# Optimization experiments

Hardware: AMD Instinct MI355X
Metric: run time of the kernel (lower is better)

Reference implementation:

```python
import jax, jax.numpy as jnp
import numpy as np

K = 9  # kernel_size (knn neighbors, loop=True -> self included)

def setup_inputs() -> dict:
    key = jax.random.key(0)
    k1, k2, k3 = jax.random.split(key, 3)
    B, C, H, W = 8, 64, 32, 32
    OUT = 64
    x = jax.random.normal(k1, (B, C, H, W), dtype=jnp.float32)
    # SAGEConv params: lin_l (neighbor aggregate, with bias), lin_r (root, no bias)
    s = 1.0 / np.sqrt(C)
    W_l = jax.random.uniform(k2, (OUT, C), minval=-s, maxval=s, dtype=jnp.float32)
    b_l = jnp.zeros((OUT,), dtype=jnp.float32)
    W_r = jax.random.uniform(k3, (OUT, C), minval=-s, maxval=s, dtype=jnp.float32)
    return {"x": x, "W_l": W_l, "b_l": b_l, "W_r": W_r}

def _knn_mean(x_f, batches):
    # squared-euclidean pairwise distances [N, N], masked across batches
    sq = jnp.sum(x_f * x_f, axis=-1)
    dist = sq[:, None] + sq[None, :] - 2.0 * (x_f @ x_f.T)
    cross = batches[:, None] != batches[None, :]
    dist = jnp.where(cross, jnp.inf, dist)
    neg, idx = jax.lax.top_k(-dist, K)          # k nearest (self included, dist 0)
    valid = (neg != -jnp.inf).astype(x_f.dtype)  # handle degenerate last-batch node
    nbr = x_f[idx] * valid[..., None]            # [N, K, C]
    return nbr.sum(axis=1) / valid.sum(axis=1, keepdims=True)

def reference(x, W_l, b_l, W_r):
    B, C, H, Wd = x.shape
    N = B * H * Wd
    x_f = x.transpose(0, 2, 3, 1).reshape(N, C)  # flat_nodes: [B*H*W, C]
    # torch.linspace(0, B, steps=N).to(int64): truncation of i*B/(N-1)
    batches = jnp.linspace(0.0, float(B), N).astype(jnp.int32)
    mean_nbr = _knn_mean(x_f, batches)
    # SAGEConv: lin_l(mean_j x_j) + lin_r(x_i)
    return mean_nbr @ W_l.T + b_l + x_f @ W_r.T
```

## Files before the change

### kernel.cpp

```cpp
#include <hip/hip_runtime.h>
#include <cstdint>
#include <cstddef>


__global__ __launch_bounds__(256, 2) void k_all(const float* __restrict__ x,
                                                const float* __restrict__ Wl,
                                                const float* __restrict__ bl,
                                                const float* __restrict__ Wr,
                                                float* __restrict__ out) {
  __shared__ float SH[8320];
  float4* Asf4 = (float4*)SH;

  int bi = (int)blockIdx.x, t = threadIdx.x;
  int lane = t & 63, w = t >> 6;
  int n0 = bi << 4;
  int s = (n0 >= 7168) ? 7168 : (n0 & ~1023);
  const float* xb = x + ((size_t)(s >> 10) << 16);
  const float* xrow = x + ((size_t)(n0 >> 10) << 16) + (n0 & 1023);

  {
    int ch = t >> 2, g = t & 3;
    Asf4[t] = *(const float4*)&xrow[((size_t)ch << 10) + (g << 2)];
  }
  __syncthreads();

  float4 av = Asf4[(lane << 2) + w];

  float acc[4][16];
  float sqa[16];
#pragma unroll
  for (int r = 0; r < 4; ++r)
#pragma unroll
    for (int j = 0; j < 16; ++j) acc[r][j] = 0.f;
#pragma unroll
  for (int j = 0; j < 16; ++j) sqa[j] = 0.f;

  const float* xl = xb + (lane << 2);
#pragma unroll 4
  for (int ch = 0; ch < 64; ++ch) {
    float4 a4 = Asf4[(ch << 2) + w];
    const float* xc = xl + ((size_t)ch << 10);
    float4 b0 = *(const float4*)&xc[0];
    float4 b1 = *(const float4*)&xc[256];
    float4 b2 = *(const float4*)&xc[512];
    float4 b3 = *(const float4*)&xc[768];
    float bv[16] = {b0.x, b0.y, b0.z, b0.w, b1.x, b1.y, b1.z, b1.w,
                    b2.x, b2.y, b2.z, b2.w, b3.x, b3.y, b3.z, b3.w};
    float ar[4] = {a4.x, a4.y, a4.z, a4.w};
#pragma unroll
    for (int j = 0; j < 16; ++j) {
      sqa[j] = fmaf(bv[j], bv[j], sqa[j]);
      acc[0][j] = fmaf(ar[0], bv[j], acc[0][j]);
      acc[1][j] = fmaf(ar[1], bv[j], acc[1][j]);
      acc[2][j] = fmaf(ar[2], bv[j], acc[2][j]);
      acc[3][j] = fmaf(ar[3], bv[j], acc[3][j]);
    }
  }

  float msum[4];
  int cnt[4];
#pragma unroll 4
  for (int rr = 0; rr < 4; ++rr) {
    int n = n0 + (w << 2) + rr;
    float xself = (rr == 0) ? av.x : (rr == 1) ? av.y : (rr == 2) ? av.z : av.w;
    if (n == 8191) {
      msum[rr] = xself;
      cnt[rr] = 1;
    } else {
      cnt[rr] = 9;
      int ln = n - s;
      int slot_o = ((ln >> 8) << 2) | (ln & 3);
      float sv = sqa[0];
#pragma unroll
      for (int j = 1; j < 16; ++j) sv = (slot_o == j) ? sqa[j] : sv;
      float si = __int_as_float(
          __builtin_amdgcn_readlane(__float_as_int(sv), (ln & 255) >> 2));
      bool mlast = (n >= 7168);
      unsigned long long cand[16];
#pragma unroll
      for (int q = 0; q < 4; ++q) {
#pragma unroll
        for (int e = 0; e < 4; ++e) {
          float d = (si + sqa[(q << 2) + e]) - 2.f * acc[rr][(q << 2) + e];
          unsigned u = __float_as_uint(d);
          u = (u & 0x80000000u) ? ~u : (u | 0x80000000u);
          unsigned jj = (unsigned)((q << 8) + (lane << 2) + e);
          cand[(q << 2) + e] = ((unsigned long long)u << 32) | jj;
        }
      }
      if (mlast && lane == 63) cand[15] = ~0ull;
      unsigned long long m1 = cand[0], m2 = cand[1];
      if (m2 < m1) { unsigned long long tt = m1; m1 = m2; m2 = tt; }
#pragma unroll
      for (int q = 2; q < 16; ++q) {
        unsigned long long c = cand[q];
        unsigned long long lo = (c < m1) ? c : m1;
        unsigned long long hi = (c < m1) ? m1 : c;
        m2 = (hi < m2) ? hi : m2;
        m1 = lo;
      }
      unsigned long long lm = m1;
      unsigned rmask = 0;
      bool stale = false;
      unsigned jloc[9];
#pragma unroll
      for (int kk = 0; kk < 9; ++kk) {
        unsigned long long g = lm;
#pragma unroll
        for (int off = 32; off; off >>= 1) {
          unsigned ghi = __shfl_xor((unsigned)(g >> 32), off, 64);
          unsigned glo = __shfl_xor((unsigned)g, off, 64);
          unsigned long long o = ((unsigned long long)ghi << 32) | glo;
          g = (o < g) ? o : g;
        }
        jloc[kk] = (unsigned)g & 1023u;
        if (lm == g) {
          unsigned slot = (((unsigned)g >> 6) & 12u) | ((unsigned)g & 3u);
          rmask |= 1u << slot;
          if (!stale) { lm = m2; stale = true; }
          else {
            unsigned long long best = ~0ull;
#pragma unroll
            for (int q = 0; q < 16; ++q) {
              bool alive = ((rmask >> q) & 1u) == 0u;
              unsigned long long c = cand[q];
              best = (alive && c < best) ? c : best;
            }
            lm = best;
          }
        }
      }
      const float* gx = xb + ((size_t)lane << 10);
      float g0 = gx[jloc[0]], g1 = gx[jloc[1]], g2 = gx[jloc[2]];
      float g3 = gx[jloc[3]], g4 = gx[jloc[4]], g5 = gx[jloc[5]];
      float g6 = gx[jloc[6]], g7 = gx[jloc[7]], g8 = gx[jloc[8]];
      msum[rr] = (((g0 + g1) + (g2 + g3)) + ((g4 + g5) + (g6 + g7))) + g8;
    }
  }
  __syncthreads();

#pragma unroll
  for (int i = 0; i < 16; ++i) {
    int lin = t + (i << 8);
    int o = lin >> 6, c = lin & 63;
    SH[o * 65 + c] = Wl[lin];
    SH[4160 + o * 65 + c] = Wr[lin];
  }
  __syncthreads();

  float bias = bl[lane];
  float ms[4];
#pragma unroll
  for (int rr = 0; rr < 4; ++rr)
    ms[rr] = (cnt[rr] == 9) ? msum[rr] * (1.f / 9.f) : msum[rr];
  float xr[4] = {av.x, av.y, av.z, av.w};
  float accL[4] = {0.f, 0.f, 0.f, 0.f};
  float accR[4] = {0.f, 0.f, 0.f, 0.f};
#pragma unroll
  for (int c = 0; c < 64; ++c) {
    float wlc = SH[lane * 65 + c];
    float wrc = SH[4160 + lane * 65 + c];
#pragma unroll
    for (int rr = 0; rr < 4; ++rr) {
      float mc = __int_as_float(__builtin_amdgcn_readlane(__float_as_int(ms[rr]), c));
      float xc = __int_as_float(__builtin_amdgcn_readlane(__float_as_int(xr[rr]), c));
      accL[rr] = fmaf(mc, wlc, accL[rr]);
      accR[rr] = fmaf(xc, wrc, accR[rr]);
    }
  }
#pragma unroll
  for (int rr = 0; rr < 4; ++rr)
    __builtin_nontemporal_store(accL[rr] + accR[rr] + bias,
                                &out[((size_t)(n0 + (w << 2) + rr) << 6) + lane]);
}

extern "C" void kernel_launch(void* const* d_in, const int* in_sizes, int n_in,
                              void* d_out, int out_size, void* d_ws, size_t ws_size,
                              hipStream_t stream) {
  const float* x  = (const float*)d_in[0];
  const float* Wl = (const float*)d_in[1];
  const float* bl = (const float*)d_in[2];
  const float* Wr = (const float*)d_in[3];
  float* out = (float*)d_out;
  (void)d_ws; (void)ws_size;

  k_all<<<dim3(512), 256, 0, stream>>>(x, Wl, bl, Wr, out);
}
```

Before: 107.0 us.

## Double-buffer distance loads and interleave top-k shuffle reductions across four rows

The distance GEMM loop now double-buffers global loads of two channels at a time in registers, so loads for the next pair overlap the FMAs on the current pair. The top-k selection handles all four rows together: the nine shuffle reductions of the four rows are interleaved to add instruction-level parallelism. Candidate keys are recomputed on demand instead of being kept in a 16-entry array, and the special-case row is handled by a select at the end. The cost is higher register pressure and extra recomputation in the rescan path.

```diff
diff --git a/kernel.cpp b/kernel.cpp
--- a/kernel.cpp
+++ b/kernel.cpp
@@ -2,6 +2,8 @@
 #include <cstdint>
 #include <cstddef>
 
+
+typedef unsigned long long u64;
 
 __global__ __launch_bounds__(256, 2) void k_all(const float* __restrict__ x,
                                                 const float* __restrict__ Wl,
@@ -36,106 +38,169 @@
   for (int j = 0; j < 16; ++j) sqa[j] = 0.f;
 
   const float* xl = xb + (lane << 2);
-#pragma unroll 4
-  for (int ch = 0; ch < 64; ++ch) {
-    float4 a4 = Asf4[(ch << 2) + w];
-    const float* xc = xl + ((size_t)ch << 10);
-    float4 b0 = *(const float4*)&xc[0];
-    float4 b1 = *(const float4*)&xc[256];
-    float4 b2 = *(const float4*)&xc[512];
-    float4 b3 = *(const float4*)&xc[768];
-    float bv[16] = {b0.x, b0.y, b0.z, b0.w, b1.x, b1.y, b1.z, b1.w,
-                    b2.x, b2.y, b2.z, b2.w, b3.x, b3.y, b3.z, b3.w};
-    float ar[4] = {a4.x, a4.y, a4.z, a4.w};
-#pragma unroll
-    for (int j = 0; j < 16; ++j) {
-      sqa[j] = fmaf(bv[j], bv[j], sqa[j]);
-      acc[0][j] = fmaf(ar[0], bv[j], acc[0][j]);
-      acc[1][j] = fmaf(ar[1], bv[j], acc[1][j]);
-      acc[2][j] = fmaf(ar[2], bv[j], acc[2][j]);
-      acc[3][j] = fmaf(ar[3], bv[j], acc[3][j]);
+
+#define LOADB(BUF, CH) do {                                                  \
+    const float* xc0_ = xl + ((size_t)(CH) << 10);                           \
+    const float* xc1_ = xl + ((size_t)((CH) + 1) << 10);                     \
+    BUF[0] = *(const float4*)&xc0_[0];   BUF[1] = *(const float4*)&xc0_[256];\
+    BUF[2] = *(const float4*)&xc0_[512]; BUF[3] = *(const float4*)&xc0_[768];\
+    BUF[4] = *(const float4*)&xc1_[0];   BUF[5] = *(const float4*)&xc1_[256];\
+    BUF[6] = *(const float4*)&xc1_[512]; BUF[7] = *(const float4*)&xc1_[768];\
+  } while (0)
+
+#define FMA2(BUF, CH) do {                                                   \
+    float4 a0_ = Asf4[((CH) << 2) + w];                                      \
+    float4 a1_ = Asf4[(((CH) + 1) << 2) + w];                                \
+    float bv0_[16] = {BUF[0].x, BUF[0].y, BUF[0].z, BUF[0].w,                \
+                      BUF[1].x, BUF[1].y, BUF[1].z, BUF[1].w,                \
+                      BUF[2].x, BUF[2].y, BUF[2].z, BUF[2].w,                \
+                      BUF[3].x, BUF[3].y, BUF[3].z, BUF[3].w};               \
+    _Pragma("unroll")                                                        \
+    for (int j_ = 0; j_ < 16; ++j_) {                                        \
+      float bv_ = bv0_[j_];                                                  \
+      sqa[j_] = fmaf(bv_, bv_, sqa[j_]);                                     \
+      acc[0][j_] = fmaf(a0_.x, bv_, acc[0][j_]);                             \
+      acc[1][j_] = fmaf(a0_.y, bv_, acc[1][j_]);                             \
+      acc[2][j_] = fmaf(a0_.z, bv_, acc[2][j_]);                             \
+      acc[3][j_] = fmaf(a0_.w, bv_, acc[3][j_]);                             \
+    }                                                                        \
+    float bv1_[16] = {BUF[4].x, BUF[4].y, BUF[4].z, BUF[4].w,                \
+                      BUF[5].x, BUF[5].y, BUF[5].z, BUF[5].w,                \
+                      BUF[6].x, BUF[6].y, BUF[6].z, BUF[6].w,                \
+                      BUF[7].x, BUF[7].y, BUF[7].z, BUF[7].w};               \
+    _Pragma("unroll")                                                        \
+    for (int j_ = 0; j_ < 16; ++j_) {                                        \
+      float bv_ = bv1_[j_];                                                  \
+      sqa[j_] = fmaf(bv_, bv_, sqa[j_]);                                     \
+      acc[0][j_] = fmaf(a1_.x, bv_, acc[0][j_]);                             \
+      acc[1][j_] = fmaf(a1_.y, bv_, acc[1][j_]);                             \
+      acc[2][j_] = fmaf(a1_.z, bv_, acc[2][j_]);                             \
+      acc[3][j_] = fmaf(a1_.w, bv_, acc[3][j_]);                             \
+    }                                                                        \
+  } while (0)
+
+  {
+    float4 bA[8], bB[8];
+    LOADB(bA, 0);
+#pragma unroll 1
+    for (int g = 0; g < 16; ++g) {
+      int c0 = g << 2;
+      LOADB(bB, c0 + 2);
+      FMA2(bA, c0);
+      if (g < 15) LOADB(bA, c0 + 4);
+      FMA2(bB, c0 + 2);
     }
   }
 
-  float msum[4];
-  int cnt[4];
-#pragma unroll 4
+#define MKKEY(RR, Q, E, SI, MLAST) ({                                        \
+    float dd_ = ((SI) + sqa[((Q) << 2) + (E)]) - 2.f * acc[RR][((Q) << 2) + (E)]; \
+    unsigned uu_ = __float_as_uint(dd_);                                     \
+    uu_ = (uu_ & 0x80000000u) ? ~uu_ : (uu_ | 0x80000000u);                  \
+    u64 kk_ = ((u64)uu_ << 32) | (unsigned)(((Q) << 8) + (lane << 2) + (E)); \
+    ((MLAST) && lane == 63 && (Q) == 3 && (E) == 3) ? ~0ull : kk_;           \
+  })
+
+  int nrow[4];
+  bool sel[4];
+  float si4[4];
+#pragma unroll
   for (int rr = 0; rr < 4; ++rr) {
     int n = n0 + (w << 2) + rr;
-    float xself = (rr == 0) ? av.x : (rr == 1) ? av.y : (rr == 2) ? av.z : av.w;
-    if (n == 8191) {
-      msum[rr] = xself;
-      cnt[rr] = 1;
-    } else {
-      cnt[rr] = 9;
-      int ln = n - s;
-      int slot_o = ((ln >> 8) << 2) | (ln & 3);
-      float sv = sqa[0];
-#pragma unroll
-      for (int j = 1; j < 16; ++j) sv = (slot_o == j) ? sqa[j] : sv;
-      float si = __int_as_float(
-          __builtin_amdgcn_readlane(__float_as_int(sv), (ln & 255) >> 2));
-      bool mlast = (n >= 7168);
-      unsigned long long cand[16];
-#pragma unroll
-      for (int q = 0; q < 4; ++q) {
-#pragma unroll
-        for (int e = 0; e < 4; ++e) {
-          float d = (si + sqa[(q << 2) + e]) - 2.f * acc[rr][(q << 2) + e];
-          unsigned u = __float_as_uint(d);
-          u = (u & 0x80000000u) ? ~u : (u | 0x80000000u);
-          unsigned jj = (unsigned)((q << 8) + (lane << 2) + e);
-          cand[(q << 2) + e] = ((unsigned long long)u << 32) | jj;
-        }
-      }
-      if (mlast && lane == 63) cand[15] = ~0ull;
-      unsigned long long m1 = cand[0], m2 = cand[1];
-      if (m2 < m1) { unsigned long long tt = m1; m1 = m2; m2 = tt; }
-#pragma unroll
-      for (int q = 2; q < 16; ++q) {
-        unsigned long long c = cand[q];
-        unsigned long long lo = (c < m1) ? c : m1;
-        unsigned long long hi = (c < m1) ? m1 : c;
+    nrow[rr] = n;
+    sel[rr] = (n != 8191);
+    int ln = n - s;
+    int slot_o = ((ln >> 8) << 2) | (ln & 3);
+    float sv = sqa[0];
+#pragma unroll
+    for (int j = 1; j < 16; ++j) sv = (slot_o == j) ? sqa[j] : sv;
+    si4[rr] = __int_as_float(
+        __builtin_amdgcn_readlane(__float_as_int(sv), (ln & 255) >> 2));
+  }
+
+  u64 m1v[4], m2v[4];
+#pragma unroll
+  for (int rr = 0; rr < 4; ++rr) {
+    bool mlast = (nrow[rr] >= 7168);
+    float si = si4[rr];
+    u64 m1 = MKKEY(rr, 0, 0, si, mlast);
+    u64 m2 = MKKEY(rr, 0, 1, si, mlast);
+    if (m2 < m1) { u64 tt = m1; m1 = m2; m2 = tt; }
+#pragma unroll
+    for (int q = 0; q < 4; ++q)
+#pragma unroll
+      for (int e = 0; e < 4; ++e) {
+        if (q == 0 && e < 2) continue;
+        u64 c = MKKEY(rr, q, e, si, mlast);
+        u64 lo = (c < m1) ? c : m1;
+        u64 hi = (c < m1) ? m1 : c;
         m2 = (hi < m2) ? hi : m2;
         m1 = lo;
       }
-      unsigned long long lm = m1;
-      unsigned rmask = 0;
-      bool stale = false;
-      unsigned jloc[9];
-#pragma unroll
-      for (int kk = 0; kk < 9; ++kk) {
-        unsigned long long g = lm;
-#pragma unroll
-        for (int off = 32; off; off >>= 1) {
-          unsigned ghi = __shfl_xor((unsigned)(g >> 32), off, 64);
-          unsigned glo = __shfl_xor((unsigned)g, off, 64);
-          unsigned long long o = ((unsigned long long)ghi << 32) | glo;
-          g = (o < g) ? o : g;
-        }
-        jloc[kk] = (unsigned)g & 1023u;
-        if (lm == g) {
-          unsigned slot = (((unsigned)g >> 6) & 12u) | ((unsigned)g & 3u);
-          rmask |= 1u << slot;
-          if (!stale) { lm = m2; stale = true; }
-          else {
-            unsigned long long best = ~0ull;
-#pragma unroll
-            for (int q = 0; q < 16; ++q) {
-              bool alive = ((rmask >> q) & 1u) == 0u;
-              unsigned long long c = cand[q];
-              best = (alive && c < best) ? c : best;
-            }
-            lm = best;
-          }
-        }
-      }
-      const float* gx = xb + ((size_t)lane << 10);
-      float g0 = gx[jloc[0]], g1 = gx[jloc[1]], g2 = gx[jloc[2]];
-      float g3 = gx[jloc[3]], g4 = gx[jloc[4]], g5 = gx[jloc[5]];
-      float g6 = gx[jloc[6]], g7 = gx[jloc[7]], g8 = gx[jloc[8]];
-      msum[rr] = (((g0 + g1) + (g2 + g3)) + ((g4 + g5) + (g6 + g7))) + g8;
+    m1v[rr] = m1; m2v[rr] = m2;
+  }
+
+#define RESCAN(RR) do {                                                      \
+    bool mlast_ = (nrow[RR] >= 7168);                                        \
+    float si_ = si4[RR];                                                     \
+    u64 best_ = ~0ull;                                                       \
+    _Pragma("unroll")                                                        \
+    for (int q_ = 0; q_ < 4; ++q_)                                           \
+      _Pragma("unroll")                                                      \
+      for (int e_ = 0; e_ < 4; ++e_) {                                       \
+        u64 c_ = MKKEY(RR, q_, e_, si_, mlast_);                             \
+        bool alive_ = ((rmaskv[RR] >> ((q_ << 2) | e_)) & 1u) == 0u;         \
+        best_ = (alive_ && c_ < best_) ? c_ : best_;                         \
+      }                                                                      \
+    lmv[RR] = best_;                                                         \
+  } while (0)
+
+#define WINUPD(RR, G) do {                                                   \
+    jloc[RR][kk] = (unsigned)(G) & 1023u;                                    \
+    if (lmv[RR] == (G)) {                                                    \
+      unsigned slot_ = (((unsigned)(G) >> 6) & 12u) | ((unsigned)(G) & 3u);  \
+      rmaskv[RR] |= 1u << slot_;                                             \
+      if (!stalev[RR]) { lmv[RR] = m2v[RR]; stalev[RR] = true; }             \
+      else RESCAN(RR);                                                       \
+    }                                                                        \
+  } while (0)
+
+  u64 lmv[4] = {m1v[0], m1v[1], m1v[2], m1v[3]};
+  unsigned rmaskv[4] = {0u, 0u, 0u, 0u};
+  bool stalev[4] = {false, false, false, false};
+  unsigned jloc[4][9];
+#pragma unroll
+  for (int kk = 0; kk < 9; ++kk) {
+    u64 g0 = lmv[0], g1 = lmv[1], g2 = lmv[2], g3 = lmv[3];
+#pragma unroll
+    for (int off = 32; off; off >>= 1) {
+      unsigned a0 = __shfl_xor((unsigned)(g0 >> 32), off, 64);
+      unsigned b0 = __shfl_xor((unsigned)g0, off, 64);
+      unsigned a1 = __shfl_xor((unsigned)(g1 >> 32), off, 64);
+      unsigned b1 = __shfl_xor((unsigned)g1, off, 64);
+      unsigned a2 = __shfl_xor((unsigned)(g2 >> 32), off, 64);
+      unsigned b2 = __shfl_xor((unsigned)g2, off, 64);
+      unsigned a3 = __shfl_xor((unsigned)(g3 >> 32), off, 64);
+      unsigned b3 = __shfl_xor((unsigned)g3, off, 64);
+      u64 o0 = ((u64)a0 << 32) | b0;
+      u64 o1 = ((u64)a1 << 32) | b1;
+      u64 o2 = ((u64)a2 << 32) | b2;
+      u64 o3 = ((u64)a3 << 32) | b3;
+      g0 = (o0 < g0) ? o0 : g0;
+      g1 = (o1 < g1) ? o1 : g1;
+      g2 = (o2 < g2) ? o2 : g2;
+      g3 = (o3 < g3) ? o3 : g3;
     }
+    WINUPD(0, g0); WINUPD(1, g1); WINUPD(2, g2); WINUPD(3, g3);
+  }
+
+  float msum[4];
+#pragma unroll
+  for (int rr = 0; rr < 4; ++rr) {
+    const float* gx = xb + ((size_t)lane << 10);
+    float g0 = gx[jloc[rr][0]], g1 = gx[jloc[rr][1]], g2 = gx[jloc[rr][2]];
+    float g3 = gx[jloc[rr][3]], g4 = gx[jloc[rr][4]], g5 = gx[jloc[rr][5]];
+    float g6 = gx[jloc[rr][6]], g7 = gx[jloc[rr][7]], g8 = gx[jloc[rr][8]];
+    msum[rr] = (((g0 + g1) + (g2 + g3)) + ((g4 + g5) + (g6 + g7))) + g8;
   }
   __syncthreads();
 
@@ -149,11 +214,11 @@
   __syncthreads();
 
   float bias = bl[lane];
+  float xr[4] = {av.x, av.y, av.z, av.w};
   float ms[4];
 #pragma unroll
   for (int rr = 0; rr < 4; ++rr)
-    ms[rr] = (cnt[rr] == 9) ? msum[rr] * (1.f / 9.f) : msum[rr];
-  float xr[4] = {av.x, av.y, av.z, av.w};
+    ms[rr] = sel[rr] ? msum[rr] * (1.f / 9.f) : xr[rr];
   float accL[4] = {0.f, 0.f, 0.f, 0.f};
   float accR[4] = {0.f, 0.f, 0.f, 0.f};
 #pragma unroll
```

After: 117.6 us. 10.0% more time.
